# Kernel tuning notes

Measured on AMD Instinct MI355X. Metric: run time of the kernel, lower is better.

The kernel has to match this reference:

```python
import jax, jax.numpy as jnp
import numpy as np

FEATURE_SIZE = 128  # H = W = feature_size per __init__
BATCH = 8


def setup_inputs() -> dict:
    key = jax.random.key(0)
    # uniform [0,1): threshold >0.5 marks ~half the pixels as 'boundary'
    feature_map = jax.random.uniform(key, (BATCH, 1, FEATURE_SIZE, FEATURE_SIZE), dtype=jnp.float32)
    return {"feature_map": feature_map}


def reference(feature_map):
    """Distance transform: for each pixel (i,j), min Euclidean distance to any
    boundary pixel (feature_map > 0.5), where the boundary set is pooled over
    batch+channel (matching torch.where on the full tensor) and the resulting
    scalar is broadcast to every batch element (matching output[:, :, i, j] = min).
    """
    B, C, H, W = feature_map.shape
    ch = jnp.arange(H, dtype=feature_map.dtype)
    cw = jnp.arange(W, dtype=feature_map.dtype)
    dx2 = (ch[:, None] - ch[None, :]) ** 2  # [H(h), H(i)]
    dy2 = (cw[:, None] - cw[None, :]) ** 2  # [W(w), W(j)]
    # boundary positions, unioned over batch/channel (grid is batch-independent)
    mask = jnp.any(feature_map > 0.5, axis=(0, 1))  # [H, W]
    # all-pairs squared distances: axes (h, w, i, j)
    d2 = dx2[:, None, :, None] + dy2[None, :, None, :]  # [H, W, H, W]
    masked = jnp.where(mask[:, :, None, None], d2, jnp.inf)
    dist = jnp.sqrt(jnp.min(masked, axis=(0, 1)))  # [H, W]; sqrt(min)=min(sqrt)
    return jnp.broadcast_to(dist[None, None], (B, C, H, W))
```

## Files before the change

### kernel.cpp

```cpp
#include <hip/hip_runtime.h>
#include <math.h>

#define H_DIM 128
#define W_DIM 128
#define BATCH 8
#define NPIX (H_DIM * W_DIM)
#define INF_I (1 << 28)

__global__ __launch_bounds__(256) void mask_kernel(const float* __restrict__ fm,
                                                   unsigned char* __restrict__ mask) {
    const int idx4 = blockIdx.x * 256 + threadIdx.x;
    const float4* fm4 = (const float4*)fm;
    bool m0 = false, m1 = false, m2 = false, m3 = false;
    #pragma unroll
    for (int b = 0; b < BATCH; ++b) {
        float4 v = fm4[b * 4096 + idx4];
        m0 |= v.x > 0.5f;
        m1 |= v.y > 0.5f;
        m2 |= v.z > 0.5f;
        m3 |= v.w > 0.5f;
    }
    uchar4 mm;
    mm.x = (unsigned char)m0;
    mm.y = (unsigned char)m1;
    mm.z = (unsigned char)m2;
    mm.w = (unsigned char)m3;
    ((uchar4*)mask)[idx4] = mm;
}

__global__ __launch_bounds__(256) void dt_kernel(const unsigned char* __restrict__ mask,
                                                 float* __restrict__ out) {
    const int i = blockIdx.x;
    const int tid = threadIdx.x;

    __shared__ unsigned char maskS[NPIX];
    __shared__ int gpart[2][W_DIM];
    __shared__ int gS[W_DIM];
    __shared__ int bpart[2][W_DIM];
    __shared__ float distS[W_DIM];

    const float4* m4 = (const float4*)mask;
    #pragma unroll
    for (int q = 0; q < 4; ++q)
        ((float4*)maskS)[q * 256 + tid] = m4[q * 256 + tid];
    __syncthreads();

    const int w = tid & 127;
    const int half = tid >> 7;

    {
        int g = INF_I;
        const int h0 = half * 64;
        #pragma unroll 4
        for (int hh = 0; hh < 64; ++hh) {
            const int h = h0 + hh;
            const int d = i - h;
            if (maskS[h * W_DIM + w]) g = min(g, d * d);
        }
        gpart[half][w] = g;
    }
    __syncthreads();
    if (tid < W_DIM) gS[tid] = min(gpart[0][tid], gpart[1][tid]);
    __syncthreads();

    {
        const int j = w;
        int best = INF_I;
        const int w0 = half * 64;
        #pragma unroll 4
        for (int ww = 0; ww < 64; ++ww) {
            const int wc = w0 + ww;
            const int d = j - wc;
            best = min(best, gS[wc] + d * d);
        }
        bpart[half][j] = best;
    }
    __syncthreads();
    if (tid < W_DIM) {
        const int best = min(bpart[0][tid], bpart[1][tid]);
        distS[tid] = (best >= INF_I) ? INFINITY : sqrtf((float)best);
    }
    __syncthreads();

    const int j = tid & 127;
    const int bh = tid >> 7;
    const float v = distS[j];
    #pragma unroll
    for (int k = 0; k < 4; ++k) {
        const int b = bh * 4 + k;
        out[b * NPIX + i * W_DIM + j] = v;
    }
}

extern "C" void kernel_launch(void* const* d_in, const int* in_sizes, int n_in,
                              void* d_out, int out_size, void* d_ws, size_t ws_size,
                              hipStream_t stream) {
    const float* fm = (const float*)d_in[0];
    float* out = (float*)d_out;
    unsigned char* mask = (unsigned char*)d_ws;

    mask_kernel<<<16, 256, 0, stream>>>(fm, mask);
    dt_kernel<<<H_DIM, 256, 0, stream>>>(mask, out);
}
```

Measured before the change: 57.50 us.

## Fuse mask computation into distance kernel and widen blocks to 1024 threads

Removes the separate mask kernel: every block now recomputes the full boundary mask from the input directly into shared memory, which eliminates one launch and the workspace round trip. Blocks grow to 1024 threads, splitting both min-reduction passes over 8 segments of 16 instead of 2 of 64, with an 8-way combine. The cost is redundant global/L2 reads of the whole input by all 128 blocks and heavier per-block prologue.

```diff
diff --git a/kernel.cpp b/kernel.cpp
--- a/kernel.cpp
+++ b/kernel.cpp
@@ -6,90 +6,84 @@
 #define BATCH 8
 #define NPIX (H_DIM * W_DIM)
 #define INF_I (1 << 28)
+#define NT 1024
 
-__global__ __launch_bounds__(256) void mask_kernel(const float* __restrict__ fm,
-                                                   unsigned char* __restrict__ mask) {
-    const int idx4 = blockIdx.x * 256 + threadIdx.x;
-    const float4* fm4 = (const float4*)fm;
-    bool m0 = false, m1 = false, m2 = false, m3 = false;
-    #pragma unroll
-    for (int b = 0; b < BATCH; ++b) {
-        float4 v = fm4[b * 4096 + idx4];
-        m0 |= v.x > 0.5f;
-        m1 |= v.y > 0.5f;
-        m2 |= v.z > 0.5f;
-        m3 |= v.w > 0.5f;
-    }
-    uchar4 mm;
-    mm.x = (unsigned char)m0;
-    mm.y = (unsigned char)m1;
-    mm.z = (unsigned char)m2;
-    mm.w = (unsigned char)m3;
-    ((uchar4*)mask)[idx4] = mm;
-}
-
-__global__ __launch_bounds__(256) void dt_kernel(const unsigned char* __restrict__ mask,
-                                                 float* __restrict__ out) {
+__global__ __launch_bounds__(NT) void fused_dt_kernel(const float* __restrict__ fm,
+                                                      float* __restrict__ out) {
     const int i = blockIdx.x;
     const int tid = threadIdx.x;
 
     __shared__ unsigned char maskS[NPIX];
-    __shared__ int gpart[2][W_DIM];
+    __shared__ int part[8][W_DIM];
     __shared__ int gS[W_DIM];
-    __shared__ int bpart[2][W_DIM];
     __shared__ float distS[W_DIM];
 
-    const float4* m4 = (const float4*)mask;
+    const float4* fm4 = (const float4*)fm;
     #pragma unroll
-    for (int q = 0; q < 4; ++q)
-        ((float4*)maskS)[q * 256 + tid] = m4[q * 256 + tid];
+    for (int q = 0; q < 4; ++q) {
+        const int f = q * NT + tid;
+        bool m0 = false, m1 = false, m2 = false, m3 = false;
+        #pragma unroll
+        for (int b = 0; b < BATCH; ++b) {
+            float4 v = fm4[b * 4096 + f];
+            m0 |= v.x > 0.5f;
+            m1 |= v.y > 0.5f;
+            m2 |= v.z > 0.5f;
+            m3 |= v.w > 0.5f;
+        }
+        uchar4 mm;
+        mm.x = (unsigned char)m0;
+        mm.y = (unsigned char)m1;
+        mm.z = (unsigned char)m2;
+        mm.w = (unsigned char)m3;
+        ((uchar4*)maskS)[f] = mm;
+    }
     __syncthreads();
 
-    const int w = tid & 127;
-    const int half = tid >> 7;
+    const int w   = tid & 127;
+    const int seg = tid >> 7;
 
     {
         int g = INF_I;
-        const int h0 = half * 64;
-        #pragma unroll 4
-        for (int hh = 0; hh < 64; ++hh) {
-            const int h = h0 + hh;
+        const int h0 = seg * 16;
+        #pragma unroll
+        for (int k = 0; k < 16; ++k) {
+            const int h = h0 + k;
             const int d = i - h;
             if (maskS[h * W_DIM + w]) g = min(g, d * d);
         }
-        gpart[half][w] = g;
+        part[seg][w] = g;
     }
     __syncthreads();
-    if (tid < W_DIM) gS[tid] = min(gpart[0][tid], gpart[1][tid]);
+    if (tid < W_DIM) {
+        int g = part[0][tid];
+        #pragma unroll
+        for (int s = 1; s < 8; ++s) g = min(g, part[s][tid]);
+        gS[tid] = g;
+    }
     __syncthreads();
 
     {
-        const int j = w;
         int best = INF_I;
-        const int w0 = half * 64;
-        #pragma unroll 4
-        for (int ww = 0; ww < 64; ++ww) {
-            const int wc = w0 + ww;
-            const int d = j - wc;
+        const int w0 = seg * 16;
+        #pragma unroll
+        for (int k = 0; k < 16; ++k) {
+            const int wc = w0 + k;
+            const int d = w - wc;
             best = min(best, gS[wc] + d * d);
         }
-        bpart[half][j] = best;
+        part[seg][w] = best;
     }
     __syncthreads();
     if (tid < W_DIM) {
-        const int best = min(bpart[0][tid], bpart[1][tid]);
+        int best = part[0][tid];
+        #pragma unroll
+        for (int s = 1; s < 8; ++s) best = min(best, part[s][tid]);
         distS[tid] = (best >= INF_I) ? INFINITY : sqrtf((float)best);
     }
     __syncthreads();
 
-    const int j = tid & 127;
-    const int bh = tid >> 7;
-    const float v = distS[j];
-    #pragma unroll
-    for (int k = 0; k < 4; ++k) {
-        const int b = bh * 4 + k;
-        out[b * NPIX + i * W_DIM + j] = v;
-    }
+    out[seg * NPIX + i * W_DIM + w] = distS[w];
 }
 
 extern "C" void kernel_launch(void* const* d_in, const int* in_sizes, int n_in,
@@ -97,8 +91,7 @@
                               hipStream_t stream) {
     const float* fm = (const float*)d_in[0];
     float* out = (float*)d_out;
-    unsigned char* mask = (unsigned char*)d_ws;
+    (void)d_ws; (void)ws_size;
 
-    mask_kernel<<<16, 256, 0, stream>>>(fm, mask);
-    dt_kernel<<<H_DIM, 256, 0, stream>>>(mask, out);
+    fused_dt_kernel<<<H_DIM, NT, 0, stream>>>(fm, out);
 }
```

New measurement: 58.23 us. About the same (+1.3%).
